# Kernel optimization log

Hardware: AMD Instinct MI355X
Metric: run time of the kernel (lower is better)

## Reference

```python
import jax, jax.numpy as jnp
import numpy as np

EPS = 0.5


def setup_inputs() -> dict:
    key = jax.random.key(0)
    k_x, k_e, k_w1, k_b1, k_w2, k_b2 = jax.random.split(key, 6)
    N, E = 100000, 600000
    D_IN, D_HID, D_OUT = 128, 256, 128
    x = jax.random.normal(k_x, (N, D_IN), dtype=jnp.float32)
    edge_index = jax.random.randint(k_e, (2, E), 0, N, dtype=jnp.int64)
    # nn.Linear params: weight [out, in], bias [out]; kaiming-uniform-ish init
    lim1 = 1.0 / np.sqrt(D_IN)
    W1 = jax.random.uniform(k_w1, (D_HID, D_IN), minval=-lim1, maxval=lim1, dtype=jnp.float32)
    b1 = jax.random.uniform(k_b1, (D_HID,), minval=-lim1, maxval=lim1, dtype=jnp.float32)
    lim2 = 1.0 / np.sqrt(D_HID)
    W2 = jax.random.uniform(k_w2, (D_OUT, D_HID), minval=-lim2, maxval=lim2, dtype=jnp.float32)
    b2 = jax.random.uniform(k_b2, (D_OUT,), minval=-lim2, maxval=lim2, dtype=jnp.float32)
    return {"x": x, "edge_index": edge_index, "W1": W1, "b1": b1, "W2": W2, "b2": b2}


def reference(x, edge_index, W1, b1, W2, b2):
    # gather both endpoint features per edge and sum: [E, D_IN]
    s = x[edge_index[0]] + x[edge_index[1]]
    # 2-layer MLP: Linear -> ReLU -> Linear
    h = jax.nn.relu(s @ W1.T + b1)          # [E, D_HID]
    edge_attr = h @ W2.T + b2               # [E, D_OUT]
    return EPS * edge_attr
```

## Files before the change

### kernel.cpp

```cpp
#include <hip/hip_runtime.h>
#include <hip/hip_bf16.h>

#define EDGES 600000
#define DIN 128
#define DHID 256
#define DOUT 128

#define NCHUNK 37500
#define NBLK 512
#define THREADS 512
#define STRIDE 4096

#define W2_OFF 65536
#define B1_OFF 131072
#define B2_OFF 132096
#define LDS_BYTES 132608

typedef __attribute__((ext_vector_type(4))) float floatx4;
typedef __attribute__((ext_vector_type(4))) short shortx4;
typedef __attribute__((ext_vector_type(8))) short shortx8;

__device__ inline unsigned short f2bf_rne(float f) {
    union { float f; unsigned u; } v; v.f = f;
    unsigned r = v.u + 0x7FFFu + ((v.u >> 16) & 1u);
    return (unsigned short)(r >> 16);
}

__global__ __launch_bounds__(256) void prep_kernel(
        const float* __restrict__ W1, const float* __restrict__ W2,
        unsigned short* __restrict__ ws) {
    int j = blockIdx.x * 256 + threadIdx.x;
    if (j < 4096) {
        int lane = j & 63, fs = j >> 6;
        int ks = fs & 3, t = fs >> 2;
        int hid = t * 16 + (lane & 15), q = lane >> 4;
        const float* src = W1 + hid * DIN + ks * 32 + q * 8;
        shortx8 v;
        #pragma unroll
        for (int i = 0; i < 8; ++i) v[i] = (short)f2bf_rne(src[i]);
        *((shortx8*)ws + j) = v;
    } else if (j < 12288) {
        int j2 = j - 4096;
        int lane = j2 & 63, fs = j2 >> 6;
        int ot = fs & 7, t = fs >> 3;
        int o = ot * 16 + (lane & 15), q = lane >> 4;
        const float* src = W2 + o * DHID + t * 16 + q * 4;
        shortx4 v;
        #pragma unroll
        for (int i = 0; i < 4; ++i) v[i] = (short)f2bf_rne(src[i]);
        *((shortx4*)(ws + 32768) + j2) = v;
    }
}

__global__ __launch_bounds__(512, 2) void gin_kernel(
        const float* __restrict__ x, const int* __restrict__ ei,
        const float* __restrict__ b1, const float* __restrict__ b2,
        const unsigned short* __restrict__ wsw,
        float* __restrict__ out) {
    extern __shared__ char smem[];
    const int tid = threadIdx.x;
    const int lane = tid & 63, q = lane >> 4, col = lane & 15;

    const int gw = blockIdx.x * 8 + (tid >> 6);
    int ch = gw;
    {
    }
    const int e0 = ch * 16 + col;
    const int na0 = ei[e0];
    const int nb0 = ei[EDGES + e0];

    {
        const float4* gsrc = (const float4*)wsw;
        #pragma unroll 4
        for (int it = 0; it < 16; ++it) {
            const int idx = it * 512 + tid;
            float4 v = gsrc[idx];
            *(float4*)(smem + (size_t)idx * 16) = v;
        }
        if (tid < 384) {
            float v = (tid < 256) ? b1[tid] : b2[tid - 256];
            *(float*)(smem + B1_OFF + tid * 4) = v;
        }
    }

    float4 raw[16];
    {
        const float* pa = x + (size_t)na0 * DIN + q * 8;
        const float* pb = x + (size_t)nb0 * DIN + q * 8;
        #pragma unroll
        for (int ks = 0; ks < 4; ++ks) {
            raw[ks*4+0] = *(const float4*)(pa + ks*32);
            raw[ks*4+1] = *(const float4*)(pa + ks*32 + 4);
            raw[ks*4+2] = *(const float4*)(pb + ks*32);
            raw[ks*4+3] = *(const float4*)(pb + ks*32 + 4);
        }
    }
    int naN, nbN;
    {
        const int e1 = (ch + STRIDE) * 16 + col;
        naN = ei[e1];
        nbN = ei[EDGES + e1];
    }
    __syncthreads();

    const shortx8* w1l = (const shortx8*)smem + lane;
    const shortx4* w2l = (const shortx4*)(smem + W2_OFF) + lane;
    const floatx4* b1l = (const floatx4*)(smem + B1_OFF) + q;
    const floatx4* b2l = (const floatx4*)(smem + B2_OFF) + q;

    for (;;) {
        shortx8 sfrag[4];
        #pragma unroll
        for (int ks = 0; ks < 4; ++ks) {
            float4 u0 = raw[ks*4+0], u1 = raw[ks*4+1];
            float4 v0 = raw[ks*4+2], v1 = raw[ks*4+3];
            union { shortx8 s8; __hip_bfloat162 b[4]; } pk;
            pk.b[0] = __float22bfloat162_rn(make_float2(u0.x+v0.x, u0.y+v0.y));
            pk.b[1] = __float22bfloat162_rn(make_float2(u0.z+v0.z, u0.w+v0.w));
            pk.b[2] = __float22bfloat162_rn(make_float2(u1.x+v1.x, u1.y+v1.y));
            pk.b[3] = __float22bfloat162_rn(make_float2(u1.z+v1.z, u1.w+v1.w));
            sfrag[ks] = pk.s8;
        }

        const int chN = ch + STRIDE;
        const bool haveN = (chN < NCHUNK);
        if (haveN) {
            const float* pa = x + (size_t)naN * DIN + q * 8;
            const float* pb = x + (size_t)nbN * DIN + q * 8;
            #pragma unroll
            for (int ks = 0; ks < 4; ++ks) {
                raw[ks*4+0] = *(const float4*)(pa + ks*32);
                raw[ks*4+1] = *(const float4*)(pa + ks*32 + 4);
                raw[ks*4+2] = *(const float4*)(pb + ks*32);
                raw[ks*4+3] = *(const float4*)(pb + ks*32 + 4);
            }
            const int ch2 = chN + STRIDE;
            if (ch2 < NCHUNK) {
                const int e2 = ch2 * 16 + col;
                naN = ei[e2];
                nbN = ei[EDGES + e2];
            }
        }

        floatx4 acc2[8];
        #pragma unroll
        for (int ot = 0; ot < 8; ++ot) acc2[ot] = b2l[ot*4];

        #pragma unroll 1
        for (int t = 0; t < 16; ++t) {
            shortx8 a1[4];
            #pragma unroll
            for (int ks = 0; ks < 4; ++ks) a1[ks] = w1l[(t*4+ks)*64];
            floatx4 acc1 = b1l[t*4];
            #pragma unroll
            for (int ks = 0; ks < 4; ++ks)
                acc1 = __builtin_amdgcn_mfma_f32_16x16x32_bf16(a1[ks], sfrag[ks], acc1, 0, 0, 0);
            union { shortx4 s4; __hip_bfloat162 b[2]; } pk;
            pk.b[0] = __float22bfloat162_rn(make_float2(fmaxf(acc1[0], 0.f), fmaxf(acc1[1], 0.f)));
            pk.b[1] = __float22bfloat162_rn(make_float2(fmaxf(acc1[2], 0.f), fmaxf(acc1[3], 0.f)));
            const shortx4 hf = pk.s4;
            #pragma unroll
            for (int ot = 0; ot < 8; ++ot) {
                shortx4 wb = w2l[(t*8+ot)*64];
                acc2[ot] = __builtin_amdgcn_mfma_f32_16x16x16bf16_1k(wb, hf, acc2[ot], 0, 0, 0);
            }
        }

        {
            float* op = out + (size_t)(ch * 16 + col) * DOUT + q * 4;
            #pragma unroll
            for (int ot = 0; ot < 8; ++ot) {
                floatx4 v = acc2[ot] * 0.5f;
                *(floatx4*)(op + ot * 16) = v;
            }
        }

        if (!haveN) break;
        ch = chN;
    }
}

extern "C" void kernel_launch(void* const* d_in, const int* in_sizes, int n_in,
                              void* d_out, int out_size, void* d_ws, size_t ws_size,
                              hipStream_t stream) {
    const float* x  = (const float*)d_in[0];
    const int*   ei = (const int*)d_in[1];
    const float* W1 = (const float*)d_in[2];
    const float* b1 = (const float*)d_in[3];
    const float* W2 = (const float*)d_in[4];
    const float* b2 = (const float*)d_in[5];
    unsigned short* ws = (unsigned short*)d_ws;

    static bool attr_done = false;
    if (!attr_done) {
        (void)hipFuncSetAttribute((const void*)gin_kernel,
                                  hipFuncAttributeMaxDynamicSharedMemorySize,
                                  LDS_BYTES);
        attr_done = true;
    }

    prep_kernel<<<48, 256, 0, stream>>>(W1, W2, ws);
    gin_kernel<<<NBLK, THREADS, LDS_BYTES, stream>>>(x, ei, b1, b2, ws, (float*)d_out);
}
```

Measured before the change: 445.2 us.

## Double-buffer edge feature gathers two chunks ahead and use nontemporal output stores

Deepens the software pipeline to two register buffers (rawA/rawB), so each wave keeps gathers in flight two chunks ahead while the node-index loads run three chunks ahead. The loop is unrolled by two via a macro so the buffers alternate without copies. Output stores become nontemporal to reduce cache pollution. In exchange it uses 64 more VGPRs per thread for the second buffer, which may cause spills or reduce occupancy under the launch bound of 512 threads with 2 blocks.

Measured after the change: 466.5 us. 4.8% more time.

```diff
diff --git a/kernel.cpp b/kernel.cpp
--- a/kernel.cpp
+++ b/kernel.cpp
@@ -52,6 +52,72 @@
     }
 }
 
+#define GATHER(RAW, NA, NB) do {                                              \
+    const float* pa_ = x + (size_t)(NA) * DIN + q * 8;                        \
+    const float* pb_ = x + (size_t)(NB) * DIN + q * 8;                        \
+    _Pragma("unroll")                                                         \
+    for (int ks_ = 0; ks_ < 4; ++ks_) {                                       \
+        RAW[ks_*4+0] = *(const float4*)(pa_ + ks_*32);                        \
+        RAW[ks_*4+1] = *(const float4*)(pa_ + ks_*32 + 4);                    \
+        RAW[ks_*4+2] = *(const float4*)(pb_ + ks_*32);                        \
+        RAW[ks_*4+3] = *(const float4*)(pb_ + ks_*32 + 4);                    \
+    }                                                                         \
+} while (0)
+
+#define BODY(RAW, NA_USE, NB_USE, NA_SET, NB_SET, C) do {                     \
+    shortx8 sfrag[4];                                                         \
+    _Pragma("unroll")                                                         \
+    for (int ks_ = 0; ks_ < 4; ++ks_) {                                       \
+        float4 u0 = RAW[ks_*4+0], u1 = RAW[ks_*4+1];                          \
+        float4 v0 = RAW[ks_*4+2], v1 = RAW[ks_*4+3];                          \
+        union { shortx8 s8; __hip_bfloat162 b[4]; } pk;                       \
+        pk.b[0] = __float22bfloat162_rn(make_float2(u0.x+v0.x, u0.y+v0.y));   \
+        pk.b[1] = __float22bfloat162_rn(make_float2(u0.z+v0.z, u0.w+v0.w));   \
+        pk.b[2] = __float22bfloat162_rn(make_float2(u1.x+v1.x, u1.y+v1.y));   \
+        pk.b[3] = __float22bfloat162_rn(make_float2(u1.z+v1.z, u1.w+v1.w));   \
+        sfrag[ks_] = pk.s8;                                                   \
+    }                                                                         \
+    {                                                                         \
+        const int cp_ = (C) + 3*STRIDE;                                       \
+        if (cp_ < NCHUNK) {                                                   \
+            const int ep_ = cp_*16 + col;                                     \
+            NA_SET = ei[ep_]; NB_SET = ei[EDGES + ep_];                       \
+        }                                                                     \
+        const int cg_ = (C) + 2*STRIDE;                                       \
+        if (cg_ < NCHUNK) GATHER(RAW, NA_USE, NB_USE);                        \
+    }                                                                         \
+    floatx4 acc2[8];                                                          \
+    _Pragma("unroll")                                                         \
+    for (int ot = 0; ot < 8; ++ot) acc2[ot] = b2l[ot*4];                      \
+    _Pragma("unroll 1")                                                       \
+    for (int t = 0; t < 16; ++t) {                                            \
+        shortx8 a1[4];                                                        \
+        _Pragma("unroll")                                                     \
+        for (int ks_ = 0; ks_ < 4; ++ks_) a1[ks_] = w1l[(t*4+ks_)*64];        \
+        floatx4 acc1 = b1l[t*4];                                              \
+        _Pragma("unroll")                                                     \
+        for (int ks_ = 0; ks_ < 4; ++ks_)                                     \
+            acc1 = __builtin_amdgcn_mfma_f32_16x16x32_bf16(a1[ks_], sfrag[ks_], acc1, 0, 0, 0); \
+        union { shortx4 s4; __hip_bfloat162 b[2]; } pk2;                      \
+        pk2.b[0] = __float22bfloat162_rn(make_float2(fmaxf(acc1[0], 0.f), fmaxf(acc1[1], 0.f))); \
+        pk2.b[1] = __float22bfloat162_rn(make_float2(fmaxf(acc1[2], 0.f), fmaxf(acc1[3], 0.f))); \
+        const shortx4 hf = pk2.s4;                                            \
+        _Pragma("unroll")                                                     \
+        for (int ot = 0; ot < 8; ++ot) {                                      \
+            shortx4 wb = w2l[(t*8+ot)*64];                                    \
+            acc2[ot] = __builtin_amdgcn_mfma_f32_16x16x16bf16_1k(wb, hf, acc2[ot], 0, 0, 0); \
+        }                                                                     \
+    }                                                                         \
+    {                                                                         \
+        float* op_ = out + (size_t)((C)*16 + col) * DOUT + q * 4;             \
+        _Pragma("unroll")                                                     \
+        for (int ot = 0; ot < 8; ++ot) {                                      \
+            floatx4 v_ = acc2[ot] * 0.5f;                                     \
+            __builtin_nontemporal_store(v_, (floatx4*)(op_ + ot*16));         \
+        }                                                                     \
+    }                                                                         \
+} while (0)
+
 __global__ __launch_bounds__(512, 2) void gin_kernel(
         const float* __restrict__ x, const int* __restrict__ ei,
         const float* __restrict__ b1, const float* __restrict__ b2,
@@ -60,14 +126,11 @@
     extern __shared__ char smem[];
     const int tid = threadIdx.x;
     const int lane = tid & 63, q = lane >> 4, col = lane & 15;
+    const int gw = blockIdx.x * 8 + (tid >> 6);
 
-    const int gw = blockIdx.x * 8 + (tid >> 6);
     int ch = gw;
-    {
-    }
-    const int e0 = ch * 16 + col;
-    const int na0 = ei[e0];
-    const int nb0 = ei[EDGES + e0];
+    float4 rawA[16], rawB[16];
+    int naP, nbP, naQ, nbQ;
 
     {
         const float4* gsrc = (const float4*)wsw;
@@ -81,25 +144,20 @@
             float v = (tid < 256) ? b1[tid] : b2[tid - 256];
             *(float*)(smem + B1_OFF + tid * 4) = v;
         }
-    }
-
-    float4 raw[16];
-    {
-        const float* pa = x + (size_t)na0 * DIN + q * 8;
-        const float* pb = x + (size_t)nb0 * DIN + q * 8;
-        #pragma unroll
-        for (int ks = 0; ks < 4; ++ks) {
-            raw[ks*4+0] = *(const float4*)(pa + ks*32);
-            raw[ks*4+1] = *(const float4*)(pa + ks*32 + 4);
-            raw[ks*4+2] = *(const float4*)(pb + ks*32);
-            raw[ks*4+3] = *(const float4*)(pb + ks*32 + 4);
+        const int e0 = ch * 16 + col;
+        const int a0 = ei[e0], b0 = ei[EDGES + e0];
+        GATHER(rawA, a0, b0);
+        const int c1 = ch + STRIDE;
+        if (c1 < NCHUNK) {
+            const int e1 = c1 * 16 + col;
+            const int a1v = ei[e1], b1v = ei[EDGES + e1];
+            GATHER(rawB, a1v, b1v);
         }
-    }
-    int naN, nbN;
-    {
-        const int e1 = (ch + STRIDE) * 16 + col;
-        naN = ei[e1];
-        nbN = ei[EDGES + e1];
+        const int c2 = ch + 2 * STRIDE;
+        if (c2 < NCHUNK) {
+            const int e2 = c2 * 16 + col;
+            naP = ei[e2]; nbP = ei[EDGES + e2];
+        }
     }
     __syncthreads();
 
@@ -109,74 +167,11 @@
     const floatx4* b2l = (const floatx4*)(smem + B2_OFF) + q;
 
     for (;;) {
-        shortx8 sfrag[4];
-        #pragma unroll
-        for (int ks = 0; ks < 4; ++ks) {
-            float4 u0 = raw[ks*4+0], u1 = raw[ks*4+1];
-            float4 v0 = raw[ks*4+2], v1 = raw[ks*4+3];
-            union { shortx8 s8; __hip_bfloat162 b[4]; } pk;
-            pk.b[0] = __float22bfloat162_rn(make_float2(u0.x+v0.x, u0.y+v0.y));
-            pk.b[1] = __float22bfloat162_rn(make_float2(u0.z+v0.z, u0.w+v0.w));
-            pk.b[2] = __float22bfloat162_rn(make_float2(u1.x+v1.x, u1.y+v1.y));
-            pk.b[3] = __float22bfloat162_rn(make_float2(u1.z+v1.z, u1.w+v1.w));
-            sfrag[ks] = pk.s8;
-        }
-
-        const int chN = ch + STRIDE;
-        const bool haveN = (chN < NCHUNK);
-        if (haveN) {
-            const float* pa = x + (size_t)naN * DIN + q * 8;
-            const float* pb = x + (size_t)nbN * DIN + q * 8;
-            #pragma unroll
-            for (int ks = 0; ks < 4; ++ks) {
-                raw[ks*4+0] = *(const float4*)(pa + ks*32);
-                raw[ks*4+1] = *(const float4*)(pa + ks*32 + 4);
-                raw[ks*4+2] = *(const float4*)(pb + ks*32);
-                raw[ks*4+3] = *(const float4*)(pb + ks*32 + 4);
-            }
-            const int ch2 = chN + STRIDE;
-            if (ch2 < NCHUNK) {
-                const int e2 = ch2 * 16 + col;
-                naN = ei[e2];
-                nbN = ei[EDGES + e2];
-            }
-        }
-
-        floatx4 acc2[8];
-        #pragma unroll
-        for (int ot = 0; ot < 8; ++ot) acc2[ot] = b2l[ot*4];
-
-        #pragma unroll 1
-        for (int t = 0; t < 16; ++t) {
-            shortx8 a1[4];
-            #pragma unroll
-            for (int ks = 0; ks < 4; ++ks) a1[ks] = w1l[(t*4+ks)*64];
-            floatx4 acc1 = b1l[t*4];
-            #pragma unroll
-            for (int ks = 0; ks < 4; ++ks)
-                acc1 = __builtin_amdgcn_mfma_f32_16x16x32_bf16(a1[ks], sfrag[ks], acc1, 0, 0, 0);
-            union { shortx4 s4; __hip_bfloat162 b[2]; } pk;
-            pk.b[0] = __float22bfloat162_rn(make_float2(fmaxf(acc1[0], 0.f), fmaxf(acc1[1], 0.f)));
-            pk.b[1] = __float22bfloat162_rn(make_float2(fmaxf(acc1[2], 0.f), fmaxf(acc1[3], 0.f)));
-            const shortx4 hf = pk.s4;
-            #pragma unroll
-            for (int ot = 0; ot < 8; ++ot) {
-                shortx4 wb = w2l[(t*8+ot)*64];
-                acc2[ot] = __builtin_amdgcn_mfma_f32_16x16x16bf16_1k(wb, hf, acc2[ot], 0, 0, 0);
-            }
-        }
-
-        {
-            float* op = out + (size_t)(ch * 16 + col) * DOUT + q * 4;
-            #pragma unroll
-            for (int ot = 0; ot < 8; ++ot) {
-                floatx4 v = acc2[ot] * 0.5f;
-                *(floatx4*)(op + ot * 16) = v;
-            }
-        }
-
-        if (!haveN) break;
-        ch = chN;
+        BODY(rawA, naP, nbP, naQ, nbQ, ch);
+        if (ch + STRIDE >= NCHUNK) break;
+        BODY(rawB, naQ, nbQ, naP, nbP, ch + STRIDE);
+        if (ch + 2 * STRIDE >= NCHUNK) break;
+        ch += 2 * STRIDE;
     }
 }
 
```
